# Performance work log

Hardware: AMD Instinct MI355X
Metric: run time of the kernel (lower is better)

The kernel has to match this reference:

```python
import jax, jax.numpy as jnp
import numpy as np

N_NODES = 50000
N_EDGES = 800000
IN_DIM = 128
HID = 128
LATENT = 64
N_LAYERS = 3
N_GRAPHS = 256
BN_EPS = 1e-5


def setup_inputs() -> dict:
    key = jax.random.key(0)
    ks = jax.random.split(key, 12)
    x = jax.random.normal(ks[0], (N_NODES, IN_DIM), dtype=jnp.float32)
    edge_index = jax.random.randint(ks[1], (2, N_EDGES), 0, N_NODES, dtype=jnp.int32)
    batch = jnp.sort(jax.random.randint(ks[2], (N_NODES,), 0, N_GRAPHS, dtype=jnp.int32))
    s = 1.0 / np.sqrt(HID)
    # stacked per-layer SAGEConv params: lin_l (neighbor path, with bias), lin_r (root path)
    Wl = jax.random.uniform(ks[3], (N_LAYERS, HID, HID), jnp.float32, -s, s)
    bl = jax.random.uniform(ks[4], (N_LAYERS, HID), jnp.float32, -s, s)
    Wr = jax.random.uniform(ks[5], (N_LAYERS, HID, HID), jnp.float32, -s, s)
    gamma = jnp.ones((HID,), jnp.float32)
    beta = jnp.zeros((HID,), jnp.float32)
    fcW = jax.random.uniform(ks[6], (HID, LATENT), jnp.float32, -s, s)
    fcb = jax.random.uniform(ks[7], (LATENT,), jnp.float32, -s, s)
    return {"x": x, "edge_index": edge_index, "batch": batch, "Wl": Wl, "bl": bl,
            "Wr": Wr, "gamma": gamma, "beta": beta, "fcW": fcW, "fcb": fcb}


def _sage_conv(x, src, dst, Wl_i, bl_i, Wr_i):
    # mean-aggregate source features into target nodes (PyG SAGEConv, aggr='mean')
    agg = jax.ops.segment_sum(x[src], dst, num_segments=N_NODES)  # [N, D]
    cnt = jax.ops.segment_sum(jnp.ones((src.shape[0],), x.dtype), dst, num_segments=N_NODES)
    mean = agg / jnp.maximum(cnt, 1.0)[:, None]
    return mean @ Wl_i + bl_i + x @ Wr_i


def reference(x, edge_index, batch, Wl, bl, Wr, gamma, beta, fcW, fcb):
    src, dst = edge_index[0], edge_index[1]
    h = x
    for i in range(N_LAYERS):
        h = _sage_conv(h, src, dst, Wl[i], bl[i], Wr[i])
        h = jax.nn.relu(h)  # dropout: identity at inference
    # global_add_pool over graphs
    pooled = jax.ops.segment_sum(h, batch, num_segments=N_GRAPHS)  # [G, HID]
    # BatchNorm1d over the graph dimension (batch statistics)
    mu = pooled.mean(axis=0)
    var = pooled.var(axis=0)
    normed = (pooled - mu) * jax.lax.rsqrt(var + BN_EPS) * gamma + beta
    return normed @ fcW + fcb
```

## Files before the change

kernel.cpp:

```cpp
#include <hip/hip_runtime.h>
#include <cstdint>
#include <cstddef>

constexpr int HID = 128;
constexpr int LATENT = 64;
constexpr int BSHIFT = 7;
constexpr int NBUCK_MAX = 512;
constexpr int EPB = 1024;

typedef __attribute__((ext_vector_type(8))) short short8;
typedef __attribute__((ext_vector_type(4))) float f32x4;

__device__ inline unsigned short f2bf(float f) {
    unsigned u = __float_as_uint(f);
    u += 0x7fff + ((u >> 16) & 1);
    return (unsigned short)(u >> 16);
}
__device__ inline unsigned pack_bf16x2(float lo, float hi) {
    unsigned ulo = __float_as_uint(lo);
    unsigned uhi = __float_as_uint(hi);
    ulo += 0x7fff + ((ulo >> 16) & 1);
    uhi += 0x7fff + ((uhi >> 16) & 1);
    return (ulo >> 16) | (uhi & 0xffff0000u);
}

__global__ __launch_bounds__(256) void stage1_k(const int* __restrict__ dst,
                                                const float* __restrict__ x,
                                                const float* __restrict__ Wl,
                                                const float* __restrict__ Wr,
                                                int* __restrict__ partial,
                                                unsigned* __restrict__ hx2,
                                                unsigned short* __restrict__ WT,
                                                int nE, int nbuck, int ebB, int n2x) {
    if (blockIdx.x < (unsigned)ebB) {
        __shared__ int lh[NBUCK_MAX];
        for (int b = threadIdx.x; b < nbuck; b += 256) lh[b] = 0;
        __syncthreads();
        int base = blockIdx.x * EPB;
        int end = min(base + EPB, nE);
        for (int i = base + threadIdx.x; i < end; i += 256)
            atomicAdd(&lh[dst[i] >> BSHIFT], 1);
        __syncthreads();
        int* row = partial + (size_t)blockIdx.x * NBUCK_MAX;
        for (int b = threadIdx.x; b < nbuck; b += 256) row[b] = lh[b];
    } else if (blockIdx.x < (unsigned)(ebB + 384)) {
        int idx = (blockIdx.x - ebB) * 256 + threadIdx.x;
        int l = idx / (128 * 256);
        int rem = idx % (128 * 256);
        int n = rem / 256;
        int k = rem % 256;
        float v = (k < 128) ? Wl[(size_t)l * 128 * 128 + (size_t)k * 128 + n]
                            : Wr[(size_t)l * 128 * 128 + (size_t)(k - 128) * 128 + n];
        WT[idx] = f2bf(v);
    } else {
        int i = (blockIdx.x - ebB - 384) * 256 + threadIdx.x;
        if (i < n2x) {
            float2 v = ((const float2*)x)[i];
            hx2[i] = pack_bf16x2(v.x, v.y);
        }
    }
}

__global__ __launch_bounds__(256) void colscan_k(int* __restrict__ partial,
                                                 int* __restrict__ bucketTotal, int ebB) {
    int b = blockIdx.x;
    int t = threadIdx.x;
    const int CH = (ebB + 255) / 256;
    int vals[8];
    int s = 0;
    #pragma unroll
    for (int c = 0; c < 8; ++c) {
        if (c >= CH) break;
        int k = t * CH + c;
        int v = (k < ebB) ? partial[(size_t)k * NBUCK_MAX + b] : 0;
        vals[c] = v; s += v;
    }
    __shared__ int part[256];
    part[t] = s;
    __syncthreads();
    for (int d = 1; d < 256; d <<= 1) {
        int u = (t >= d) ? part[t - d] : 0;
        __syncthreads();
        if (t >= d) part[t] += u;
        __syncthreads();
    }
    int run = (t == 0) ? 0 : part[t - 1];
    #pragma unroll
    for (int c = 0; c < 8; ++c) {
        if (c >= CH) break;
        int k = t * CH + c;
        if (k < ebB) partial[(size_t)k * NBUCK_MAX + b] = run;
        run += vals[c];
    }
    if (t == 255) bucketTotal[b] = run;
}

__global__ __launch_bounds__(512) void bscan2_k(const int* __restrict__ bucketTotal,
                                                int* __restrict__ bucketStart,
                                                int* __restrict__ row_ptr,
                                                int nbuck, int nE, int nN) {
    __shared__ int part[512];
    int t = threadIdx.x;
    int v = (t < nbuck) ? bucketTotal[t] : 0;
    part[t] = v;
    __syncthreads();
    for (int d = 1; d < 512; d <<= 1) {
        int u = (t >= d) ? part[t - d] : 0;
        __syncthreads();
        if (t >= d) part[t] += u;
        __syncthreads();
    }
    if (t < nbuck) bucketStart[t] = part[t] - v;
    if (t == 0) { bucketStart[nbuck] = nE; row_ptr[nN] = nE; }
}

__global__ __launch_bounds__(256) void bplace_k(const int* __restrict__ src,
                                                const int* __restrict__ dst,
                                                const int* __restrict__ partial,
                                                const int* __restrict__ bucketStart,
                                                uint2* __restrict__ staged, int nE, int nbuck) {
    __shared__ int lh[NBUCK_MAX];
    __shared__ int lb[NBUCK_MAX];
    for (int b = threadIdx.x; b < nbuck; b += 256) lh[b] = 0;
    __syncthreads();
    int base = blockIdx.x * EPB;
    int end = min(base + EPB, nE);
    const int* myPre = partial + (size_t)blockIdx.x * NBUCK_MAX;
    for (int b = threadIdx.x; b < nbuck; b += 256)
        lb[b] = bucketStart[b] + myPre[b];
    __syncthreads();
    for (int i = base + threadIdx.x; i < end; i += 256) {
        int d = dst[i];
        int b = d >> BSHIFT;
        int loc = atomicAdd(&lh[b], 1);
        staged[lb[b] + loc] = make_uint2((unsigned)src[i], (unsigned)d);
    }
}

__global__ __launch_bounds__(256) void sort_bucket_k(const uint2* __restrict__ staged,
                                                     const int* __restrict__ bucketStart,
                                                     int* __restrict__ row_ptr,
                                                     float* __restrict__ inv,
                                                     int* __restrict__ csr_src, int nN) {
    __shared__ int cnt[128];
    __shared__ int rp[128];
    int g = blockIdx.x;
    int beg = bucketStart[g], end = bucketStart[g + 1];
    if (threadIdx.x < 128) cnt[threadIdx.x] = 0;
    __syncthreads();
    for (int i = beg + threadIdx.x; i < end; i += 256)
        atomicAdd(&cnt[staged[i].y & 127], 1);
    __syncthreads();
    if (threadIdx.x < 128) rp[threadIdx.x] = cnt[threadIdx.x];
    __syncthreads();
    #pragma unroll
    for (int d = 1; d < 128; d <<= 1) {
        int v = 0;
        if (threadIdx.x < 128 && threadIdx.x >= d) v = rp[threadIdx.x - d];
        __syncthreads();
        if (threadIdx.x < 128 && threadIdx.x >= d) rp[threadIdx.x] += v;
        __syncthreads();
    }
    if (threadIdx.x < 128) {
        int c = cnt[threadIdx.x];
        int excl = rp[threadIdx.x] - c;
        int node = (g << BSHIFT) + threadIdx.x;
        if (node < nN) {
            row_ptr[node] = beg + excl;
            inv[node] = 1.0f / fmaxf((float)c, 1.0f);
        }
        cnt[threadIdx.x] = excl;
    }
    __syncthreads();
    for (int i = beg + threadIdx.x; i < end; i += 256) {
        uint2 e = staged[i];
        int pos = atomicAdd(&cnt[e.y & 127], 1);
        csr_src[beg + pos] = (int)e.x;
    }
}

__global__ __launch_bounds__(256) void gather_k(const int* __restrict__ row_ptr,
                                                const int* __restrict__ csr_src,
                                                const float* __restrict__ inv,
                                                const uint4* __restrict__ h4,
                                                uint4* __restrict__ mean4, int nN) {
    int w = blockIdx.x * 4 + (threadIdx.x >> 6);
    if (w >= nN) return;
    int lane = threadIdx.x & 63;
    int quarter = lane >> 4;
    int col = lane & 15;
    int beg = row_ptr[w], end = row_ptr[w + 1];
    float accA[8] = {}, accB[8] = {}, accC[8] = {}, accD[8] = {};
    for (int base = beg; base < end; base += 64) {
        int navail = min(64, end - base);
        int idx = (lane < navail) ? csr_src[base + lane] : 0;
        for (int j = 0; j < navail; j += 16) {
            int e0 = j + quarter;
            int e1 = j + 4 + quarter;
            int e2 = j + 8 + quarter;
            int e3 = j + 12 + quarter;
            int s0 = __shfl(idx, min(e0, navail - 1), 64);
            int s1 = __shfl(idx, min(e1, navail - 1), 64);
            int s2 = __shfl(idx, min(e2, navail - 1), 64);
            int s3 = __shfl(idx, min(e3, navail - 1), 64);
            uint4 u0 = h4[(size_t)s0 * 16 + col];
            uint4 u1 = h4[(size_t)s1 * 16 + col];
            uint4 u2 = h4[(size_t)s2 * 16 + col];
            uint4 u3 = h4[(size_t)s3 * 16 + col];
            if (e0 < navail) {
                accA[0] += __uint_as_float(u0.x << 16); accA[1] += __uint_as_float(u0.x & 0xffff0000u);
                accA[2] += __uint_as_float(u0.y << 16); accA[3] += __uint_as_float(u0.y & 0xffff0000u);
                accA[4] += __uint_as_float(u0.z << 16); accA[5] += __uint_as_float(u0.z & 0xffff0000u);
                accA[6] += __uint_as_float(u0.w << 16); accA[7] += __uint_as_float(u0.w & 0xffff0000u);
            }
            if (e1 < navail) {
                accB[0] += __uint_as_float(u1.x << 16); accB[1] += __uint_as_float(u1.x & 0xffff0000u);
                accB[2] += __uint_as_float(u1.y << 16); accB[3] += __uint_as_float(u1.y & 0xffff0000u);
                accB[4] += __uint_as_float(u1.z << 16); accB[5] += __uint_as_float(u1.z & 0xffff0000u);
                accB[6] += __uint_as_float(u1.w << 16); accB[7] += __uint_as_float(u1.w & 0xffff0000u);
            }
            if (e2 < navail) {
                accC[0] += __uint_as_float(u2.x << 16); accC[1] += __uint_as_float(u2.x & 0xffff0000u);
                accC[2] += __uint_as_float(u2.y << 16); accC[3] += __uint_as_float(u2.y & 0xffff0000u);
                accC[4] += __uint_as_float(u2.z << 16); accC[5] += __uint_as_float(u2.z & 0xffff0000u);
                accC[6] += __uint_as_float(u2.w << 16); accC[7] += __uint_as_float(u2.w & 0xffff0000u);
            }
            if (e3 < navail) {
                accD[0] += __uint_as_float(u3.x << 16); accD[1] += __uint_as_float(u3.x & 0xffff0000u);
                accD[2] += __uint_as_float(u3.y << 16); accD[3] += __uint_as_float(u3.y & 0xffff0000u);
                accD[4] += __uint_as_float(u3.z << 16); accD[5] += __uint_as_float(u3.z & 0xffff0000u);
                accD[6] += __uint_as_float(u3.w << 16); accD[7] += __uint_as_float(u3.w & 0xffff0000u);
            }
        }
    }
    #pragma unroll
    for (int k = 0; k < 8; ++k) {
        float v = (accA[k] + accB[k]) + (accC[k] + accD[k]);
        v += __shfl_xor(v, 16, 64);
        v += __shfl_xor(v, 32, 64);
        accA[k] = v;
    }
    if (quarter == 0) {
        float iv = inv[w];
        uint4 o;
        o.x = pack_bf16x2(accA[0] * iv, accA[1] * iv);
        o.y = pack_bf16x2(accA[2] * iv, accA[3] * iv);
        o.z = pack_bf16x2(accA[4] * iv, accA[5] * iv);
        o.w = pack_bf16x2(accA[6] * iv, accA[7] * iv);
        mean4[(size_t)w * 16 + col] = o;
    }
}

__global__ __launch_bounds__(256) void sage_mfma_k(
    const unsigned short* __restrict__ mean,
    const unsigned short* __restrict__ h,
    const unsigned short* __restrict__ WT,
    const float* __restrict__ bl,
    unsigned short* __restrict__ out, int nN)
{
    __shared__ unsigned short sB[128 * 256];

    {
        int row = threadIdx.x >> 1, half = threadIdx.x & 1;
        const short8* src = (const short8*)(WT + row * 256 + half * 128);
        int sw = (row & 7) << 2;
        #pragma unroll
        for (int j = 0; j < 16; ++j) {
            int unit = half * 16 + j;
            int unit2 = unit ^ sw;
            *(short8*)(sB + row * 256 + unit2 * 8) = src[j];
        }
    }
    __syncthreads();

    const int wave = threadIdx.x >> 6;
    const int lane = threadIdx.x & 63;
    const int m = lane & 15;
    const int q = lane >> 4;
    const int row = blockIdx.x * 64 + wave * 16 + m;
    const int rowc = min(row, nN - 1);
    const int swm = (m & 7) << 2;

    f32x4 acc[8] = {};
    #pragma unroll
    for (int ks = 0; ks < 8; ++ks) {
        const unsigned short* Aptr = (ks < 4) ? mean : h;
        short8 a = *(const short8*)(Aptr + (size_t)rowc * HID + (ks & 3) * 32 + q * 8);
        #pragma unroll
        for (int t = 0; t < 8; ++t) {
            int unit2 = (ks * 4 + q) ^ swm;
            short8 b = *(const short8*)(sB + (t * 16 + m) * 256 + unit2 * 8);
            acc[t] = __builtin_amdgcn_mfma_f32_16x16x32_bf16(a, b, acc[t], 0, 0, 0);
        }
    }

    int orow_base = blockIdx.x * 64 + wave * 16 + q * 4;
    #pragma unroll
    for (int t = 0; t < 8; ++t) {
        float bias = bl[t * 16 + m];
        #pragma unroll
        for (int r = 0; r < 4; ++r) {
            int orow = orow_base + r;
            if (orow < nN) {
                float v = fmaxf(acc[t][r] + bias, 0.f);
                out[(size_t)orow * HID + t * 16 + m] = f2bf(v);
            }
        }
    }
}

__global__ __launch_bounds__(256) void pool_seg_k(const unsigned* __restrict__ h2,
                                                  const int* __restrict__ batch,
                                                  float* __restrict__ pooled, int nN) {
    int g = blockIdx.x;
    int lo = 0, hi = nN;
    while (lo < hi) { int mid = (lo + hi) >> 1; if (batch[mid] < g) lo = mid + 1; else hi = mid; }
    int beg = lo;
    hi = nN;
    while (lo < hi) { int mid = (lo + hi) >> 1; if (batch[mid] <= g) lo = mid + 1; else hi = mid; }
    int end = lo;

    int lane = threadIdx.x & 63;
    int sub  = threadIdx.x >> 6;
    float s0 = 0.f, s1 = 0.f;
    for (int i = beg + sub; i < end; i += 4) {
        unsigned u = h2[(size_t)i * 64 + lane];
        s0 += __uint_as_float(u << 16);
        s1 += __uint_as_float(u & 0xffff0000u);
    }
    __shared__ float red[4][HID];
    red[sub][2 * lane]     = s0;
    red[sub][2 * lane + 1] = s1;
    __syncthreads();
    if (sub == 0) {
        float v0 = red[0][2 * lane] + red[1][2 * lane] + red[2][2 * lane] + red[3][2 * lane];
        float v1 = red[0][2 * lane + 1] + red[1][2 * lane + 1] + red[2][2 * lane + 1] + red[3][2 * lane + 1];
        pooled[(size_t)g * HID + 2 * lane]     = v0;
        pooled[(size_t)g * HID + 2 * lane + 1] = v1;
    }
}

__global__ __launch_bounds__(1024) void bn_stats_k(const float* __restrict__ pooled,
                                                   const float* __restrict__ gamma,
                                                   const float* __restrict__ beta,
                                                   float* __restrict__ scale,
                                                   float* __restrict__ shift, int nG) {
    __shared__ float rs[8][HID], rs2[8][HID];
    int j = threadIdx.x & (HID - 1);
    int stripe = threadIdx.x >> 7;
    float s = 0.f, s2 = 0.f;
    for (int g = stripe; g < nG; g += 8) {
        float v = pooled[(size_t)g * HID + j];
        s += v; s2 += v * v;
    }
    rs[stripe][j] = s; rs2[stripe][j] = s2;
    __syncthreads();
    if (threadIdx.x < HID) {
        float S = 0.f, S2 = 0.f;
        #pragma unroll
        for (int k = 0; k < 8; ++k) { S += rs[k][j]; S2 += rs2[k][j]; }
        float invG = 1.0f / (float)nG;
        float mu = S * invG;
        float var = S2 * invG - mu * mu;
        float r = rsqrtf(var + 1e-5f) * gamma[j];
        scale[j] = r;
        shift[j] = beta[j] - mu * r;
    }
}

__global__ __launch_bounds__(LATENT) void fc_k(const float* __restrict__ pooled,
                                               const float* __restrict__ scale,
                                               const float* __restrict__ shift,
                                               const float* __restrict__ fcW,
                                               const float* __restrict__ fcb,
                                               float* __restrict__ out, int nG) {
    int g = blockIdx.x;
    int o = threadIdx.x;
    float acc = fcb[o];
    for (int j = 0; j < HID; ++j) {
        float v = pooled[(size_t)g * HID + j] * scale[j] + shift[j];
        acc += v * fcW[(size_t)j * LATENT + o];
    }
    out[(size_t)g * LATENT + o] = acc;
}

extern "C" void kernel_launch(void* const* d_in, const int* in_sizes, int n_in,
                              void* d_out, int out_size, void* d_ws, size_t ws_size,
                              hipStream_t stream) {
    const float* x     = (const float*)d_in[0];
    const int*   ei    = (const int*)d_in[1];
    const int*   batch = (const int*)d_in[2];
    const float* Wl    = (const float*)d_in[3];
    const float* bl    = (const float*)d_in[4];
    const float* Wr    = (const float*)d_in[5];
    const float* gamma = (const float*)d_in[6];
    const float* beta  = (const float*)d_in[7];
    const float* fcW   = (const float*)d_in[8];
    const float* fcb   = (const float*)d_in[9];
    float* out = (float*)d_out;

    const int nN = in_sizes[0] / HID;
    const int nE = in_sizes[1] / 2;
    const int nG = out_size / LATENT;
    const int* src = ei;
    const int* dst = ei + nE;
    const int nbuck = (nN + 127) >> BSHIFT;
    const int ebB = (nE + EPB - 1) / EPB;

    unsigned short* hx   = (unsigned short*)d_ws;
    unsigned short* B1   = hx + (size_t)nN * HID;
    unsigned short* B2   = B1 + (size_t)nN * HID;
    unsigned short* mean = B2 + (size_t)nN * HID;
    unsigned short* WT   = mean + (size_t)nN * HID;
    float* inv    = (float*)(WT + 3 * 128 * 256);
    float* pooled = inv + nN;
    float* scale  = pooled + (size_t)nG * HID;
    float* shift  = scale + HID;
    int*   row_ptr     = (int*)(shift + HID);
    int*   csr_src     = row_ptr + (nN + 1);
    int*   bucketStart = csr_src + nE;
    int*   bucketTotal = bucketStart + NBUCK_MAX + 1;
    int*   partial     = bucketTotal + NBUCK_MAX;
    uint2* staged      = (uint2*)mean;

    const int n2x = nN * HID / 2;
    const int convx_blocks = (n2x + 255) / 256;

    stage1_k<<<ebB + 384 + convx_blocks, 256, 0, stream>>>(dst, x, Wl, Wr, partial,
                                                           (unsigned*)hx, WT, nE, nbuck, ebB, n2x);
    colscan_k<<<nbuck, 256, 0, stream>>>(partial, bucketTotal, ebB);
    bscan2_k<<<1, 512, 0, stream>>>(bucketTotal, bucketStart, row_ptr, nbuck, nE, nN);
    bplace_k<<<ebB, 256, 0, stream>>>(src, dst, partial, bucketStart, staged, nE, nbuck);
    sort_bucket_k<<<nbuck, 256, 0, stream>>>(staged, bucketStart, row_ptr, inv, csr_src, nN);

    const int gather_blocks = (nN + 3) / 4;
    const int gemm_blocks = (nN + 63) / 64;

    const unsigned short* hcur = hx;
    unsigned short* outs[3] = {B1, B2, B1};
    for (int l = 0; l < 3; ++l) {
        gather_k<<<gather_blocks, 256, 0, stream>>>(row_ptr, csr_src, inv,
                                                    (const uint4*)hcur, (uint4*)mean, nN);
        sage_mfma_k<<<gemm_blocks, 256, 0, stream>>>(mean, hcur,
                                                     WT + (size_t)l * 128 * 256,
                                                     bl + (size_t)l * HID,
                                                     outs[l], nN);
        hcur = outs[l];
    }

    pool_seg_k<<<nG, 256, 0, stream>>>((const unsigned*)hcur, batch, pooled, nN);
    bn_stats_k<<<1, 1024, 0, stream>>>(pooled, gamma, beta, scale, shift, nG);
    fc_k<<<nG, LATENT, 0, stream>>>(pooled, scale, shift, fcW, fcb, out, nG);
}
```

Measured before the change: 315.4 us.

## Fuse neighbor gather and MFMA linear into one per-layer kernel

Replaces the separate gather kernel and MFMA GEMM kernel with a single kernel per layer. Each 256-thread block aggregates 16 nodes into a swizzled LDS tile, then runs the 16x128 by 128x256 product with each wave owning 32 output columns. This removes the global round trip of the mean buffer and one launch per layer. In exchange, weights are no longer staged in LDS and are read from global/L2 by every block, and each wave now walks four nodes in sequence with only two accumulator sets instead of four, which reduces memory-level parallelism in the gather.

Result: slower. 332.8 us (+5.5%).

```diff
diff --git a/kernel.cpp b/kernel.cpp
--- a/kernel.cpp
+++ b/kernel.cpp
@@ -179,131 +179,105 @@
     }
 }
 
-__global__ __launch_bounds__(256) void gather_k(const int* __restrict__ row_ptr,
-                                                const int* __restrict__ csr_src,
-                                                const float* __restrict__ inv,
-                                                const uint4* __restrict__ h4,
-                                                uint4* __restrict__ mean4, int nN) {
-    int w = blockIdx.x * 4 + (threadIdx.x >> 6);
-    if (w >= nN) return;
-    int lane = threadIdx.x & 63;
-    int quarter = lane >> 4;
-    int col = lane & 15;
-    int beg = row_ptr[w], end = row_ptr[w + 1];
-    float accA[8] = {}, accB[8] = {}, accC[8] = {}, accD[8] = {};
-    for (int base = beg; base < end; base += 64) {
-        int navail = min(64, end - base);
-        int idx = (lane < navail) ? csr_src[base + lane] : 0;
-        for (int j = 0; j < navail; j += 16) {
-            int e0 = j + quarter;
-            int e1 = j + 4 + quarter;
-            int e2 = j + 8 + quarter;
-            int e3 = j + 12 + quarter;
-            int s0 = __shfl(idx, min(e0, navail - 1), 64);
-            int s1 = __shfl(idx, min(e1, navail - 1), 64);
-            int s2 = __shfl(idx, min(e2, navail - 1), 64);
-            int s3 = __shfl(idx, min(e3, navail - 1), 64);
-            uint4 u0 = h4[(size_t)s0 * 16 + col];
-            uint4 u1 = h4[(size_t)s1 * 16 + col];
-            uint4 u2 = h4[(size_t)s2 * 16 + col];
-            uint4 u3 = h4[(size_t)s3 * 16 + col];
-            if (e0 < navail) {
-                accA[0] += __uint_as_float(u0.x << 16); accA[1] += __uint_as_float(u0.x & 0xffff0000u);
-                accA[2] += __uint_as_float(u0.y << 16); accA[3] += __uint_as_float(u0.y & 0xffff0000u);
-                accA[4] += __uint_as_float(u0.z << 16); accA[5] += __uint_as_float(u0.z & 0xffff0000u);
-                accA[6] += __uint_as_float(u0.w << 16); accA[7] += __uint_as_float(u0.w & 0xffff0000u);
-            }
-            if (e1 < navail) {
-                accB[0] += __uint_as_float(u1.x << 16); accB[1] += __uint_as_float(u1.x & 0xffff0000u);
-                accB[2] += __uint_as_float(u1.y << 16); accB[3] += __uint_as_float(u1.y & 0xffff0000u);
-                accB[4] += __uint_as_float(u1.z << 16); accB[5] += __uint_as_float(u1.z & 0xffff0000u);
-                accB[6] += __uint_as_float(u1.w << 16); accB[7] += __uint_as_float(u1.w & 0xffff0000u);
-            }
-            if (e2 < navail) {
-                accC[0] += __uint_as_float(u2.x << 16); accC[1] += __uint_as_float(u2.x & 0xffff0000u);
-                accC[2] += __uint_as_float(u2.y << 16); accC[3] += __uint_as_float(u2.y & 0xffff0000u);
-                accC[4] += __uint_as_float(u2.z << 16); accC[5] += __uint_as_float(u2.z & 0xffff0000u);
-                accC[6] += __uint_as_float(u2.w << 16); accC[7] += __uint_as_float(u2.w & 0xffff0000u);
-            }
-            if (e3 < navail) {
-                accD[0] += __uint_as_float(u3.x << 16); accD[1] += __uint_as_float(u3.x & 0xffff0000u);
-                accD[2] += __uint_as_float(u3.y << 16); accD[3] += __uint_as_float(u3.y & 0xffff0000u);
-                accD[4] += __uint_as_float(u3.z << 16); accD[5] += __uint_as_float(u3.z & 0xffff0000u);
-                accD[6] += __uint_as_float(u3.w << 16); accD[7] += __uint_as_float(u3.w & 0xffff0000u);
-            }
-        }
-    }
-    #pragma unroll
-    for (int k = 0; k < 8; ++k) {
-        float v = (accA[k] + accB[k]) + (accC[k] + accD[k]);
-        v += __shfl_xor(v, 16, 64);
-        v += __shfl_xor(v, 32, 64);
-        accA[k] = v;
-    }
-    if (quarter == 0) {
-        float iv = inv[w];
-        uint4 o;
-        o.x = pack_bf16x2(accA[0] * iv, accA[1] * iv);
-        o.y = pack_bf16x2(accA[2] * iv, accA[3] * iv);
-        o.z = pack_bf16x2(accA[4] * iv, accA[5] * iv);
-        o.w = pack_bf16x2(accA[6] * iv, accA[7] * iv);
-        mean4[(size_t)w * 16 + col] = o;
-    }
-}
-
-__global__ __launch_bounds__(256) void sage_mfma_k(
-    const unsigned short* __restrict__ mean,
+__global__ __launch_bounds__(256) void sage_layer_k(
+    const int* __restrict__ row_ptr,
+    const int* __restrict__ csr_src,
+    const float* __restrict__ inv,
+    const uint4* __restrict__ h4,
     const unsigned short* __restrict__ h,
     const unsigned short* __restrict__ WT,
     const float* __restrict__ bl,
     unsigned short* __restrict__ out, int nN)
 {
-    __shared__ unsigned short sB[128 * 256];
-
-    {
-        int row = threadIdx.x >> 1, half = threadIdx.x & 1;
-        const short8* src = (const short8*)(WT + row * 256 + half * 128);
-        int sw = (row & 7) << 2;
-        #pragma unroll
-        for (int j = 0; j < 16; ++j) {
-            int unit = half * 16 + j;
-            int unit2 = unit ^ sw;
-            *(short8*)(sB + row * 256 + unit2 * 8) = src[j];
-        }
-    }
-    __syncthreads();
-
+    __shared__ unsigned short meanS[16 * 128];
     const int wave = threadIdx.x >> 6;
     const int lane = threadIdx.x & 63;
-    const int m = lane & 15;
-    const int q = lane >> 4;
-    const int row = blockIdx.x * 64 + wave * 16 + m;
-    const int rowc = min(row, nN - 1);
-    const int swm = (m & 7) << 2;
-
-    f32x4 acc[8] = {};
+    const int quarter = lane >> 4;
+    const int col = lane & 15;
+    const int nb = blockIdx.x * 16;
+
+    for (int ii = 0; ii < 4; ++ii) {
+        int i = wave * 4 + ii;
+        int n = nb + i;
+        float accA[8] = {}, accB[8] = {};
+        if (n < nN) {
+            int beg = row_ptr[n], end = row_ptr[n + 1];
+            for (int base = beg; base < end; base += 64) {
+                int navail = min(64, end - base);
+                int idx = (lane < navail) ? csr_src[base + lane] : 0;
+                for (int j = 0; j < navail; j += 8) {
+                    int e0 = j + quarter;
+                    int e1 = j + 4 + quarter;
+                    int s0 = __shfl(idx, min(e0, navail - 1), 64);
+                    int s1 = __shfl(idx, min(e1, navail - 1), 64);
+                    uint4 u0 = h4[(size_t)s0 * 16 + col];
+                    uint4 u1 = h4[(size_t)s1 * 16 + col];
+                    if (e0 < navail) {
+                        accA[0] += __uint_as_float(u0.x << 16); accA[1] += __uint_as_float(u0.x & 0xffff0000u);
+                        accA[2] += __uint_as_float(u0.y << 16); accA[3] += __uint_as_float(u0.y & 0xffff0000u);
+                        accA[4] += __uint_as_float(u0.z << 16); accA[5] += __uint_as_float(u0.z & 0xffff0000u);
+                        accA[6] += __uint_as_float(u0.w << 16); accA[7] += __uint_as_float(u0.w & 0xffff0000u);
+                    }
+                    if (e1 < navail) {
+                        accB[0] += __uint_as_float(u1.x << 16); accB[1] += __uint_as_float(u1.x & 0xffff0000u);
+                        accB[2] += __uint_as_float(u1.y << 16); accB[3] += __uint_as_float(u1.y & 0xffff0000u);
+                        accB[4] += __uint_as_float(u1.z << 16); accB[5] += __uint_as_float(u1.z & 0xffff0000u);
+                        accB[6] += __uint_as_float(u1.w << 16); accB[7] += __uint_as_float(u1.w & 0xffff0000u);
+                    }
+                }
+            }
+        }
+        #pragma unroll
+        for (int k = 0; k < 8; ++k) {
+            float v = accA[k] + accB[k];
+            v += __shfl_xor(v, 16, 64);
+            v += __shfl_xor(v, 32, 64);
+            accA[k] = v;
+        }
+        if (quarter == 0) {
+            float iv = inv[min(n, nN - 1)];
+            uint4 o;
+            o.x = pack_bf16x2(accA[0] * iv, accA[1] * iv);
+            o.y = pack_bf16x2(accA[2] * iv, accA[3] * iv);
+            o.z = pack_bf16x2(accA[4] * iv, accA[5] * iv);
+            o.w = pack_bf16x2(accA[6] * iv, accA[7] * iv);
+            *(uint4*)(meanS + i * 128 + ((col ^ i) & 15) * 8) = o;
+        }
+    }
+    __syncthreads();
+
+    const int m = col;
+    const int q = quarter;
+    const int rowc = min(nb + m, nN - 1);
+
+    f32x4 acc[2] = {};
     #pragma unroll
     for (int ks = 0; ks < 8; ++ks) {
-        const unsigned short* Aptr = (ks < 4) ? mean : h;
-        short8 a = *(const short8*)(Aptr + (size_t)rowc * HID + (ks & 3) * 32 + q * 8);
+        short8 a;
+        if (ks < 4) {
+            int unit = ks * 4 + q;
+            a = *(const short8*)(meanS + m * 128 + ((unit ^ m) & 15) * 8);
+        } else {
+            a = *(const short8*)(h + (size_t)rowc * HID + (ks - 4) * 32 + q * 8);
+        }
         #pragma unroll
-        for (int t = 0; t < 8; ++t) {
-            int unit2 = (ks * 4 + q) ^ swm;
-            short8 b = *(const short8*)(sB + (t * 16 + m) * 256 + unit2 * 8);
+        for (int t = 0; t < 2; ++t) {
+            int ncol = wave * 32 + t * 16 + m;
+            short8 b = *(const short8*)(WT + (size_t)ncol * 256 + (ks * 4 + q) * 8);
             acc[t] = __builtin_amdgcn_mfma_f32_16x16x32_bf16(a, b, acc[t], 0, 0, 0);
         }
     }
 
-    int orow_base = blockIdx.x * 64 + wave * 16 + q * 4;
     #pragma unroll
-    for (int t = 0; t < 8; ++t) {
-        float bias = bl[t * 16 + m];
+    for (int t = 0; t < 2; ++t) {
+        int ocol = wave * 32 + t * 16 + m;
+        float bias = bl[ocol];
         #pragma unroll
         for (int r = 0; r < 4; ++r) {
-            int orow = orow_base + r;
+            int orow = nb + q * 4 + r;
             if (orow < nN) {
                 float v = fmaxf(acc[t][r] + bias, 0.f);
-                out[(size_t)orow * HID + t * 16 + m] = f2bf(v);
+                out[(size_t)orow * HID + ocol] = f2bf(v);
             }
         }
     }
@@ -410,8 +384,8 @@
     unsigned short* hx   = (unsigned short*)d_ws;
     unsigned short* B1   = hx + (size_t)nN * HID;
     unsigned short* B2   = B1 + (size_t)nN * HID;
-    unsigned short* mean = B2 + (size_t)nN * HID;
-    unsigned short* WT   = mean + (size_t)nN * HID;
+    unsigned short* spare= B2 + (size_t)nN * HID;
+    unsigned short* WT   = spare + (size_t)nN * HID;
     float* inv    = (float*)(WT + 3 * 128 * 256);
     float* pooled = inv + nN;
     float* scale  = pooled + (size_t)nG * HID;
@@ -421,7 +395,7 @@
     int*   bucketStart = csr_src + nE;
     int*   bucketTotal = bucketStart + NBUCK_MAX + 1;
     int*   partial     = bucketTotal + NBUCK_MAX;
-    uint2* staged      = (uint2*)mean;
+    uint2* staged      = (uint2*)spare;
 
     const int n2x = nN * HID / 2;
     const int convx_blocks = (n2x + 255) / 256;
@@ -433,18 +407,16 @@
     bplace_k<<<ebB, 256, 0, stream>>>(src, dst, partial, bucketStart, staged, nE, nbuck);
     sort_bucket_k<<<nbuck, 256, 0, stream>>>(staged, bucketStart, row_ptr, inv, csr_src, nN);
 
-    const int gather_blocks = (nN + 3) / 4;
-    const int gemm_blocks = (nN + 63) / 64;
+    const int layer_blocks = (nN + 15) / 16;
 
     const unsigned short* hcur = hx;
     unsigned short* outs[3] = {B1, B2, B1};
     for (int l = 0; l < 3; ++l) {
-        gather_k<<<gather_blocks, 256, 0, stream>>>(row_ptr, csr_src, inv,
-                                                    (const uint4*)hcur, (uint4*)mean, nN);
-        sage_mfma_k<<<gemm_blocks, 256, 0, stream>>>(mean, hcur,
-                                                     WT + (size_t)l * 128 * 256,
-                                                     bl + (size_t)l * HID,
-                                                     outs[l], nN);
+        sage_layer_k<<<layer_blocks, 256, 0, stream>>>(row_ptr, csr_src, inv,
+                                                       (const uint4*)hcur, hcur,
+                                                       WT + (size_t)l * 128 * 256,
+                                                       bl + (size_t)l * HID,
+                                                       outs[l], nN);
         hcur = outs[l];
     }
 
```
